# Kernel tuning notes

Measured on AMD Instinct MI355X. Metric: run time of the kernel, lower is better.

The kernel has to match this reference:

```python
import jax, jax.numpy as jnp
import numpy as np

B, S, D = 4, 2048, 512
H, DK, DV = 8, 64, 64
DFF = 2048
LN_EPS = 1e-5


def _layernorm(x, g, b):
    mu = jnp.mean(x, axis=-1, keepdims=True)
    var = jnp.mean(jnp.square(x - mu), axis=-1, keepdims=True)
    return (x - mu) * jax.lax.rsqrt(var + LN_EPS) * g + b


def setup_inputs() -> dict:
    key = jax.random.key(0)
    ks = jax.random.split(key, 9)
    def xavier(k, shape):
        fan_out, fan_in = shape
        std = np.sqrt(2.0 / (fan_in + fan_out))
        return jax.random.normal(k, shape, jnp.float32) * std
    GELU_GAIN = 1.85
    return {
        "x": jax.random.normal(ks[0], (B, S, D), jnp.float32),
        "attention_mask": jax.random.randint(ks[1], (B, S), 0, 2).astype(bool),
        "Wq": xavier(ks[2], (H * DK, D)),
        "Wk": xavier(ks[3], (H * DK, D)),
        "Wv": xavier(ks[4], (H * DV, D)),
        "Wp": xavier(ks[5], (D, H * DV)),
        "W1": xavier(ks[6], (DFF, D)) * GELU_GAIN,
        "b1": jnp.zeros((DFF,), jnp.float32),
        "W2": xavier(ks[7], (D, DFF)),
        "b2": jnp.zeros((D,), jnp.float32),
        "ln1_g": jnp.ones((D,), jnp.float32),
        "ln1_b": jnp.zeros((D,), jnp.float32),
        "ln2_g": jnp.ones((D,), jnp.float32),
        "ln2_b": jnp.zeros((D,), jnp.float32),
    }


def reference(x, attention_mask, Wq, Wk, Wv, Wp, W1, b1, W2, b2,
              ln1_g, ln1_b, ln2_g, ln2_b):
    b, s, d = x.shape
    residual = x
    q = (x @ Wq.T).reshape(b, s, H, DK)  # [B,S,H,DK]
    k = (x @ Wk.T).reshape(b, s, H, DK)
    v = (x @ Wv.T).reshape(b, s, H, DV)
    score = jnp.einsum("bshd,bthd->bhst", q, k) * (DK ** -0.5)  # [B,H,S,S]
    # subtractive mask: score -= 100 * not(mask)
    score = score - 100.0 * (~attention_mask)[:, None, None, :].astype(score.dtype)
    p = jax.nn.softmax(score, axis=-1)
    ctx = jnp.einsum("bhst,bthd->bshd", p, v).reshape(b, s, H * DV)
    att = ctx @ Wp.T  # dropout p=0.1 is identity in eval
    h = _layernorm(att + residual, ln1_g, ln1_b)
    ff = jax.nn.gelu(h @ W1.T + b1, approximate=False) @ W2.T + b2
    out = _layernorm(ff + h, ln2_g, ln2_b)
    return out
```

## Files before the change

kernel.cpp:

```cpp
#include <hip/hip_runtime.h>
#include <cstdint>
#include <cstddef>

#define B_ 4
#define S_ 2048
#define D_ 512
#define H_ 8
#define DK_ 64
#define DFF_ 2048

using s16x8  = __attribute__((ext_vector_type(8))) short;
using bf16x8 = __attribute__((ext_vector_type(8))) __bf16;
using f32x4  = __attribute__((ext_vector_type(4))) float;

__device__ __forceinline__ short f2bf(float f) {
  unsigned u = __builtin_bit_cast(unsigned, f);
  u += 0x7FFFu + ((u >> 16) & 1u);
  return (short)(u >> 16);
}
__device__ __forceinline__ float bf2f(short s) {
  unsigned u = ((unsigned)(unsigned short)s) << 16;
  return __builtin_bit_cast(float, u);
}

__device__ __forceinline__ void gl2lds16(const void* g, void* l) {
  __builtin_amdgcn_global_load_lds(
      (const __attribute__((address_space(1))) void*)g,
      (__attribute__((address_space(3))) void*)l, 16, 0, 0);
}

__global__ __launch_bounds__(256)
void cvt_all(const float* __restrict__ x, const float* __restrict__ Wq,
             const float* __restrict__ Wk, const float* __restrict__ Wv,
             const float* __restrict__ Wp, const float* __restrict__ W1,
             const float* __restrict__ W2,
             short* __restrict__ xb, short* __restrict__ wqkv,
             short* __restrict__ wp, short* __restrict__ w1, short* __restrict__ w2) {
  int blk = blockIdx.x;
  const float* src; short* dst; int off;
  if (blk < 4096)      { src = x;  dst = xb;            off = blk; }
  else if (blk < 4352) { src = Wq; dst = wqkv;          off = blk - 4096; }
  else if (blk < 4608) { src = Wk; dst = wqkv + 262144; off = blk - 4352; }
  else if (blk < 4864) { src = Wv; dst = wqkv + 524288; off = blk - 4608; }
  else if (blk < 5120) { src = Wp; dst = wp;            off = blk - 4864; }
  else if (blk < 6144) { src = W1; dst = w1;            off = blk - 5120; }
  else                 { src = W2; dst = w2;            off = blk - 6144; }
  int i = (off * 256 + threadIdx.x) * 4;
  float4 v = *(const float4*)(src + i);
  *(short4*)(dst + i) = make_short4(f2bf(v.x), f2bf(v.y), f2bf(v.z), f2bf(v.w));
}

__global__ __launch_bounds__(256) void mask_detect(const unsigned* __restrict__ m,
                                                   unsigned* __restrict__ flag) {
  int i = blockIdx.x * 256 + threadIdx.x;
  unsigned v = m[i];
  if (v) atomicOr(flag, v);
}

__global__ __launch_bounds__(256) void mask_convert(const void* __restrict__ m,
                                                    const unsigned* __restrict__ flag,
                                                    float* __restrict__ mb) {
  int i = blockIdx.x * 256 + threadIdx.x;
  unsigned f = *flag;
  int v;
  if ((f & ~1u) == 0u)            v = ((const int*)m)[i];
  else if (f == 0x3F800000u)      v = (((const float*)m)[i] != 0.0f);
  else                            v = ((const unsigned char*)m)[i];
  mb[i] = v ? 0.0f : -100.0f;
}

constexpr int BM = 128, BN = 128, BK = 32;

template <int MODE>
__global__ __launch_bounds__(256)
void gemm_bt(const short* __restrict__ A, const short* __restrict__ B,
             int M, int N, int K,
             const float* __restrict__ aux1,
             void* __restrict__ out0, void* __restrict__ out1, void* __restrict__ out2) {
  __shared__ alignas(16) short As[BM][BK];
  __shared__ alignas(16) short Bs[BN][BK];

  const int tid  = threadIdx.x;
  const int lane = tid & 63;
  const int wave = tid >> 6;
  const int quad = lane >> 4;
  const int l16  = lane & 15;
  const int wm   = (wave >> 1) * 64;
  const int wn   = (wave & 1) * 64;
  const int bm   = blockIdx.x * BM;
  const int bn   = blockIdx.y * BN;

  const short* Ag = A + (size_t)(bm + wave * 32 + (lane >> 2)) * K + (lane & 3) * 8;
  const short* Bg = B + (size_t)(bn + wave * 32 + (lane >> 2)) * K + (lane & 3) * 8;
  short* AsW = &As[wave * 32][0];
  short* BsW = &Bs[wave * 32][0];
  const size_t row16 = (size_t)16 * K;

  f32x4 acc[4][4] = {};

  for (int k0 = 0; k0 < K; k0 += BK) {
    gl2lds16(Ag + k0,          AsW);
    gl2lds16(Ag + k0 + row16,  AsW + 16 * BK);
    gl2lds16(Bg + k0,          BsW);
    gl2lds16(Bg + k0 + row16,  BsW + 16 * BK);
    __syncthreads();

    bf16x8 a[4], b[4];
#pragma unroll
    for (int i = 0; i < 4; ++i)
      a[i] = __builtin_bit_cast(bf16x8, *(const s16x8*)&As[wm + i * 16 + l16][quad * 8]);
#pragma unroll
    for (int j = 0; j < 4; ++j)
      b[j] = __builtin_bit_cast(bf16x8, *(const s16x8*)&Bs[wn + j * 16 + l16][quad * 8]);
#pragma unroll
    for (int i = 0; i < 4; ++i)
#pragma unroll
      for (int j = 0; j < 4; ++j)
        acc[i][j] = __builtin_amdgcn_mfma_f32_16x16x32_bf16(a[i], b[j], acc[i][j], 0, 0, 0);
    __syncthreads();
  }

#pragma unroll
  for (int i = 0; i < 4; ++i) {
    const int m0 = bm + wm + i * 16 + quad * 4;
#pragma unroll
    for (int j = 0; j < 4; ++j) {
      const int n = bn + wn + j * 16 + l16;
      if constexpr (MODE == 0) {
        const int bb = m0 >> 11, ss0 = m0 & 2047;
        if (n < 512) {
          short4 pk = make_short4(f2bf(acc[i][j][0] * 0.125f), f2bf(acc[i][j][1] * 0.125f),
                                  f2bf(acc[i][j][2] * 0.125f), f2bf(acc[i][j][3] * 0.125f));
          *(short4*)((short*)out0 +
              ((((size_t)bb * H_ + (n >> 6)) * 64 + (n & 63)) * S_ + ss0)) = pk;
        } else if (n >= 1024) {
          const int nn = n - 1024;
          short4 pk = make_short4(f2bf(acc[i][j][0]), f2bf(acc[i][j][1]),
                                  f2bf(acc[i][j][2]), f2bf(acc[i][j][3]));
          *(short4*)((short*)out2 +
              ((((size_t)bb * H_ + (nn >> 6)) * 64 + (nn & 63)) * S_ + ss0)) = pk;
        } else {
          const int nn = n - 512;
          const int hh = nn >> 6, dd = nn & 63;
          const size_t rowb = ((size_t)bb * H_ + hh) * S_ + ss0;
#pragma unroll
          for (int rr = 0; rr < 4; ++rr)
            ((short*)out1)[(rowb + rr) * 64 + dd] = f2bf(acc[i][j][rr]);
        }
      } else {
#pragma unroll
        for (int rr = 0; rr < 4; ++rr) {
          float t = acc[i][j][rr] + aux1[n];
          float gl = 0.5f * t * (1.0f + erff(t * 0.70710678118f));
          ((short*)out0)[(size_t)(m0 + rr) * N + n] = f2bf(gl);
        }
      }
    }
  }
}

__global__ __launch_bounds__(128)
void gemm_bt2_sk(const short* __restrict__ A, const short* __restrict__ B,
                 int M, int N, int K, float* __restrict__ outp) {
  __shared__ alignas(16) short As[128][32];
  __shared__ alignas(16) short Bs[64][32];

  const int tid  = threadIdx.x;
  const int lane = tid & 63;
  const int wave = tid >> 6;
  const int quad = lane >> 4;
  const int l16  = lane & 15;
  const int wm   = wave * 64;
  const int bm   = blockIdx.x * 128;
  const int bn   = blockIdx.y * 64;
  const int Kh   = K >> 1;
  const int koff = blockIdx.z * Kh;

  const int srow = wave * 16 + (lane >> 2);
  const int scol = (lane & 3) * 8;
  const short* Ag = A + (size_t)(bm + srow) * K + koff + scol;
  const short* Bg = B + (size_t)(bn + srow) * K + koff + scol;
  short* AsW = &As[wave * 16][0];
  short* BsW = &Bs[wave * 16][0];
  const size_t row32 = (size_t)32 * K;

  f32x4 acc[4][4] = {};

  for (int k0 = 0; k0 < Kh; k0 += 32) {
    gl2lds16(Ag + k0,              AsW);
    gl2lds16(Ag + k0 + row32,      AsW + 32 * 32);
    gl2lds16(Ag + k0 + 2 * row32,  AsW + 64 * 32);
    gl2lds16(Ag + k0 + 3 * row32,  AsW + 96 * 32);
    gl2lds16(Bg + k0,              BsW);
    gl2lds16(Bg + k0 + row32,      BsW + 32 * 32);
    __syncthreads();

    bf16x8 a[4], b[4];
#pragma unroll
    for (int i = 0; i < 4; ++i)
      a[i] = __builtin_bit_cast(bf16x8, *(const s16x8*)&As[wm + i * 16 + l16][quad * 8]);
#pragma unroll
    for (int j = 0; j < 4; ++j)
      b[j] = __builtin_bit_cast(bf16x8, *(const s16x8*)&Bs[j * 16 + l16][quad * 8]);
#pragma unroll
    for (int i = 0; i < 4; ++i)
#pragma unroll
      for (int j = 0; j < 4; ++j)
        acc[i][j] = __builtin_amdgcn_mfma_f32_16x16x32_bf16(a[i], b[j], acc[i][j], 0, 0, 0);
    __syncthreads();
  }

  float* dst = outp + (size_t)blockIdx.z * M * N;
#pragma unroll
  for (int i = 0; i < 4; ++i) {
    const int m0 = bm + wm + i * 16 + quad * 4;
#pragma unroll
    for (int j = 0; j < 4; ++j) {
      const int n = bn + j * 16 + l16;
#pragma unroll
      for (int rr = 0; rr < 4; ++rr)
        dst[(size_t)(m0 + rr) * N + n] = acc[i][j][rr];
    }
  }
}

__global__ __launch_bounds__(256)
void flash_attn_mfma(const short* __restrict__ QTg, const short* __restrict__ Kb,
                     const short* __restrict__ Vtg, const float* __restrict__ maskbias,
                     short* __restrict__ ctxb) {
  __shared__ alignas(16) short Ks[64][72];
  __shared__ alignas(16) short Vt[64][72];
  __shared__ alignas(16) short Ps[4][32][72];
  __shared__ alignas(16) float mrow[S_];

  const int b = blockIdx.z, h = blockIdx.y;
  const int tid = threadIdx.x;
  const int w = tid >> 6, lane = tid & 63;
  const int quad = lane >> 4, l16 = lane & 15;
  const size_t base  = ((size_t)(b * H_ + h)) * S_ * DK_;
  const size_t baseT = ((size_t)(b * H_ + h)) * DK_ * S_;
  const int q0 = blockIdx.x * 128;

  {
    const float4* mp = (const float4*)(maskbias + (size_t)b * S_);
    ((float4*)mrow)[tid]       = mp[tid];
    ((float4*)mrow)[tid + 256] = mp[tid + 256];
  }

  bf16x8 qa[2][2];
#pragma unroll
  for (int st = 0; st < 2; ++st) {
    const int q = q0 + w * 32 + st * 16 + l16;
#pragma unroll
    for (int c = 0; c < 2; ++c) {
      s16x8 t;
#pragma unroll
      for (int j = 0; j < 8; ++j)
        t[j] = QTg[baseT + (size_t)(c * 32 + quad * 8 + j) * S_ + q];
      qa[st][c] = __builtin_bit_cast(bf16x8, t);
    }
  }

  f32x4 Oc[2][4] = {};
  float li[2][4] = {};

  const int r = tid >> 2, c16 = (tid & 3) * 16;
  const short* kp = Kb  + base  + (size_t)r * 64 + c16;
  const short* vp = Vtg + baseT + (size_t)r * S_ + c16;

  s16x8 kr0 = *(const s16x8*)(kp);
  s16x8 kr1 = *(const s16x8*)(kp + 8);
  s16x8 vr0 = *(const s16x8*)(vp);
  s16x8 vr1 = *(const s16x8*)(vp + 8);

  for (int t0 = 0; t0 < S_; t0 += 64) {
    __syncthreads();
    *(s16x8*)&Ks[r][c16]     = kr0;
    *(s16x8*)&Ks[r][c16 + 8] = kr1;
    *(s16x8*)&Vt[r][c16]     = vr0;
    *(s16x8*)&Vt[r][c16 + 8] = vr1;
    __syncthreads();

    if (t0 + 64 < S_) {
      kr0 = *(const s16x8*)(kp + (size_t)(t0 + 64) * 64);
      kr1 = *(const s16x8*)(kp + (size_t)(t0 + 64) * 64 + 8);
      vr0 = *(const s16x8*)(vp + t0 + 64);
      vr1 = *(const s16x8*)(vp + t0 + 64 + 8);
    }

    f32x4 sc[2][4] = {};
#pragma unroll
    for (int c = 0; c < 2; ++c) {
#pragma unroll
      for (int jt = 0; jt < 4; ++jt) {
        bf16x8 kb = __builtin_bit_cast(bf16x8,
            *(const s16x8*)&Ks[jt * 16 + l16][c * 32 + quad * 8]);
        sc[0][jt] = __builtin_amdgcn_mfma_f32_16x16x32_bf16(qa[0][c], kb, sc[0][jt], 0, 0, 0);
        sc[1][jt] = __builtin_amdgcn_mfma_f32_16x16x32_bf16(qa[1][c], kb, sc[1][jt], 0, 0, 0);
      }
    }

    float mb4[4];
#pragma unroll
    for (int jt = 0; jt < 4; ++jt) mb4[jt] = mrow[t0 + jt * 16 + l16];
#pragma unroll
    for (int st = 0; st < 2; ++st) {
#pragma unroll
      for (int jt = 0; jt < 4; ++jt) {
#pragma unroll
        for (int rr = 0; rr < 4; ++rr) {
          float p = __expf(sc[st][jt][rr] + mb4[jt]);
          unsigned u = __builtin_bit_cast(unsigned, p) & 0xFFFF0000u;
          li[st][rr] += __builtin_bit_cast(float, u);
          Ps[w][st * 16 + quad * 4 + rr][jt * 16 + l16] = (short)(u >> 16);
        }
      }
    }

#pragma unroll
    for (int c = 0; c < 2; ++c) {
      bf16x8 pa0 = __builtin_bit_cast(bf16x8,
          *(const s16x8*)&Ps[w][l16][c * 32 + quad * 8]);
      bf16x8 pa1 = __builtin_bit_cast(bf16x8,
          *(const s16x8*)&Ps[w][16 + l16][c * 32 + quad * 8]);
#pragma unroll
      for (int dt = 0; dt < 4; ++dt) {
        bf16x8 vb = __builtin_bit_cast(bf16x8,
            *(const s16x8*)&Vt[dt * 16 + l16][c * 32 + quad * 8]);
        Oc[0][dt] = __builtin_amdgcn_mfma_f32_16x16x32_bf16(pa0, vb, Oc[0][dt], 0, 0, 0);
        Oc[1][dt] = __builtin_amdgcn_mfma_f32_16x16x32_bf16(pa1, vb, Oc[1][dt], 0, 0, 0);
      }
    }
  }

#pragma unroll
  for (int st = 0; st < 2; ++st) {
#pragma unroll
    for (int rr = 0; rr < 4; ++rr) {
      float l = li[st][rr];
#pragma unroll
      for (int m = 1; m < 16; m <<= 1) l += __shfl_xor(l, m);
      float inv = 1.f / l;
      const size_t row = (size_t)b * S_ + q0 + w * 32 + st * 16 + quad * 4 + rr;
#pragma unroll
      for (int dt = 0; dt < 4; ++dt)
        ctxb[row * (H_ * DK_) + h * 64 + dt * 16 + l16] = f2bf(Oc[st][dt][rr] * inv);
    }
  }
}

__global__ __launch_bounds__(256)
void ln_fused(const float* __restrict__ p0, const float* __restrict__ p1,
              const float* __restrict__ xres, const short* __restrict__ hres,
              const float* __restrict__ bias,
              const float* __restrict__ g, const float* __restrict__ bb,
              float* __restrict__ out32, short* __restrict__ outb) {
  const int wave = threadIdx.x >> 6, lane = threadIdx.x & 63;
  const int token = blockIdx.x * 4 + wave;
  const size_t off = (size_t)token * D_;
  const int c = lane * 8;

  float v[8];
  {
    float4 a0 = *(const float4*)(p0 + off + c);
    float4 a1 = *(const float4*)(p0 + off + c + 4);
    float4 b0 = *(const float4*)(p1 + off + c);
    float4 b1 = *(const float4*)(p1 + off + c + 4);
    v[0]=a0.x+b0.x; v[1]=a0.y+b0.y; v[2]=a0.z+b0.z; v[3]=a0.w+b0.w;
    v[4]=a1.x+b1.x; v[5]=a1.y+b1.y; v[6]=a1.z+b1.z; v[7]=a1.w+b1.w;
  }
  if (xres) {
    float4 x0 = *(const float4*)(xres + off + c);
    float4 x1 = *(const float4*)(xres + off + c + 4);
    v[0]+=x0.x; v[1]+=x0.y; v[2]+=x0.z; v[3]+=x0.w;
    v[4]+=x1.x; v[5]+=x1.y; v[6]+=x1.z; v[7]+=x1.w;
  }
  if (hres) {
    short4 h0 = *(const short4*)(hres + off + c);
    short4 h1 = *(const short4*)(hres + off + c + 4);
    v[0]+=bf2f(h0.x); v[1]+=bf2f(h0.y); v[2]+=bf2f(h0.z); v[3]+=bf2f(h0.w);
    v[4]+=bf2f(h1.x); v[5]+=bf2f(h1.y); v[6]+=bf2f(h1.z); v[7]+=bf2f(h1.w);
  }
  if (bias) {
    float4 c0 = *(const float4*)(bias + c);
    float4 c1 = *(const float4*)(bias + c + 4);
    v[0]+=c0.x; v[1]+=c0.y; v[2]+=c0.z; v[3]+=c0.w;
    v[4]+=c1.x; v[5]+=c1.y; v[6]+=c1.z; v[7]+=c1.w;
  }

  float sum = 0.f;
#pragma unroll
  for (int i = 0; i < 8; ++i) sum += v[i];
#pragma unroll
  for (int m = 1; m < 64; m <<= 1) sum += __shfl_xor(sum, m);
  float mu = sum * (1.0f / D_);
  float vs = 0.f;
#pragma unroll
  for (int i = 0; i < 8; ++i) { v[i] -= mu; vs += v[i] * v[i]; }
#pragma unroll
  for (int m = 1; m < 64; m <<= 1) vs += __shfl_xor(vs, m);
  float rstd = rsqrtf(vs * (1.0f / D_) + 1e-5f);
#pragma unroll
  for (int i = 0; i < 8; ++i) {
    float val = v[i] * rstd * g[c + i] + bb[c + i];
    if (out32) out32[off + c + i] = val;
    if (outb)  outb[off + c + i] = f2bf(val);
  }
}

constexpr size_t OFF_XB   = 0;
constexpr size_t OFF_WQKV = 8388608;
constexpr size_t OFF_WP   = 9961472;
constexpr size_t OFF_W1   = 10485760;
constexpr size_t OFF_W2   = 12582912;
constexpr size_t OFF_QT   = 14680064;
constexpr size_t OFF_K    = 23068672;
constexpr size_t OFF_VT   = 31457280;
constexpr size_t OFF_CTX  = 39845888;
constexpr size_t OFF_P0   = 48234496;
constexpr size_t OFF_P1   = 65011712;
constexpr size_t OFF_HB   = 81788928;
constexpr size_t OFF_FF1  = 14680064;
constexpr size_t OFF_MB   = 90177536;
constexpr size_t OFF_FLAG = 90210304;
constexpr size_t WS_NEED  = 90210308;

extern "C" void kernel_launch(void* const* d_in, const int* in_sizes, int n_in,
                              void* d_out, int out_size, void* d_ws, size_t ws_size,
                              hipStream_t stream) {
  if (ws_size < WS_NEED) return;

  const float* x    = (const float*)d_in[0];
  const void*  msk  = d_in[1];
  const float* Wq   = (const float*)d_in[2];
  const float* Wk   = (const float*)d_in[3];
  const float* Wv   = (const float*)d_in[4];
  const float* Wp   = (const float*)d_in[5];
  const float* W1   = (const float*)d_in[6];
  const float* b1   = (const float*)d_in[7];
  const float* W2   = (const float*)d_in[8];
  const float* b2   = (const float*)d_in[9];
  const float* ln1g = (const float*)d_in[10];
  const float* ln1b = (const float*)d_in[11];
  const float* ln2g = (const float*)d_in[12];
  const float* ln2b = (const float*)d_in[13];

  char* ws = (char*)d_ws;
  short* xb    = (short*)(ws + OFF_XB);
  short* wqkv  = (short*)(ws + OFF_WQKV);
  short* Wpb   = (short*)(ws + OFF_WP);
  short* W1b   = (short*)(ws + OFF_W1);
  short* W2b   = (short*)(ws + OFF_W2);
  short* QTb   = (short*)(ws + OFF_QT);
  short* Kbh   = (short*)(ws + OFF_K);
  short* VTb   = (short*)(ws + OFF_VT);
  short* ctxb  = (short*)(ws + OFF_CTX);
  float* p0    = (float*)(ws + OFF_P0);
  short* hb    = (short*)(ws + OFF_HB);
  short* ff1b  = (short*)(ws + OFF_FF1);
  float* mbias = (float*)(ws + OFF_MB);
  unsigned* flag = (unsigned*)(ws + OFF_FLAG);

  hipMemsetAsync(flag, 0, 4, stream);
  mask_detect<<<8, 256, 0, stream>>>((const unsigned*)msk, flag);
  mask_convert<<<32, 256, 0, stream>>>(msk, flag, mbias);

  cvt_all<<<7168, 256, 0, stream>>>(x, Wq, Wk, Wv, Wp, W1, W2,
                                    xb, wqkv, Wpb, W1b, W2b);

  gemm_bt<0><<<dim3(64, 12), 256, 0, stream>>>(xb, wqkv, 8192, 1536, 512,
                                               nullptr, QTb, Kbh, VTb);

  flash_attn_mfma<<<dim3(S_ / 128, H_, B_), 256, 0, stream>>>(QTb, Kbh, VTb, mbias, ctxb);

  gemm_bt2_sk<<<dim3(64, 8, 2), 128, 0, stream>>>(ctxb, Wpb, 8192, 512, 512, p0);

  ln_fused<<<2048, 256, 0, stream>>>(p0, p0 + (size_t)8192 * 512, x, nullptr, nullptr,
                                     ln1g, ln1b, nullptr, hb);

  gemm_bt<2><<<dim3(64, 16), 256, 0, stream>>>(hb, W1b, 8192, 2048, 512,
                                               b1, ff1b, nullptr, nullptr);

  gemm_bt2_sk<<<dim3(64, 8, 2), 128, 0, stream>>>(ff1b, W2b, 8192, 512, 2048, p0);

  ln_fused<<<2048, 256, 0, stream>>>(p0, p0 + (size_t)8192 * 512, nullptr, hb, b2,
                                     ln2g, ln2b, (float*)d_out, nullptr);
}
```

Before: 340.8 us.

## Widen GEMM K-tile with XOR-swizzled LDS and unify split-K GEMMs; fuse mask kernels

Measured after the change: 325.0 us. 1.05x faster.

```diff
diff --git a/kernel.cpp b/kernel.cpp
--- a/kernel.cpp
+++ b/kernel.cpp
@@ -50,26 +50,26 @@
   *(short4*)(dst + i) = make_short4(f2bf(v.x), f2bf(v.y), f2bf(v.z), f2bf(v.w));
 }
 
-__global__ __launch_bounds__(256) void mask_detect(const unsigned* __restrict__ m,
-                                                   unsigned* __restrict__ flag) {
-  int i = blockIdx.x * 256 + threadIdx.x;
-  unsigned v = m[i];
-  if (v) atomicOr(flag, v);
-}
-
-__global__ __launch_bounds__(256) void mask_convert(const void* __restrict__ m,
-                                                    const unsigned* __restrict__ flag,
-                                                    float* __restrict__ mb) {
-  int i = blockIdx.x * 256 + threadIdx.x;
-  unsigned f = *flag;
-  int v;
-  if ((f & ~1u) == 0u)            v = ((const int*)m)[i];
-  else if (f == 0x3F800000u)      v = (((const float*)m)[i] != 0.0f);
-  else                            v = ((const unsigned char*)m)[i];
-  mb[i] = v ? 0.0f : -100.0f;
-}
-
-constexpr int BM = 128, BN = 128, BK = 32;
+__global__ __launch_bounds__(256)
+void mask_all(const void* __restrict__ m, float* __restrict__ mb) {
+  __shared__ unsigned red[4];
+  const unsigned* mw = (const unsigned*)m;
+  const int t = threadIdx.x;
+  unsigned v = 0;
+#pragma unroll
+  for (int i = 0; i < 8; ++i) v |= mw[t + i * 256];
+#pragma unroll
+  for (int s = 1; s < 64; s <<= 1) v |= __shfl_xor(v, s);
+  if ((t & 63) == 0) red[t >> 6] = v;
+  __syncthreads();
+  unsigned f = red[0] | red[1] | red[2] | red[3];
+  int i = blockIdx.x * 256 + t;
+  int val;
+  if ((f & ~1u) == 0u)            val = ((const int*)m)[i];
+  else if (f == 0x3F800000u)      val = (((const float*)m)[i] != 0.0f);
+  else                            val = ((const unsigned char*)m)[i];
+  mb[i] = val ? 0.0f : -100.0f;
+}
 
 template <int MODE>
 __global__ __launch_bounds__(256)
@@ -77,8 +77,8 @@
              int M, int N, int K,
              const float* __restrict__ aux1,
              void* __restrict__ out0, void* __restrict__ out1, void* __restrict__ out2) {
-  __shared__ alignas(16) short As[BM][BK];
-  __shared__ alignas(16) short Bs[BN][BK];
+  __shared__ alignas(16) short As[128][64];
+  __shared__ alignas(16) short Bs[128][64];
 
   const int tid  = threadIdx.x;
   const int lane = tid & 63;
@@ -87,36 +87,47 @@
   const int l16  = lane & 15;
   const int wm   = (wave >> 1) * 64;
   const int wn   = (wave & 1) * 64;
-  const int bm   = blockIdx.x * BM;
-  const int bn   = blockIdx.y * BN;
-
-  const short* Ag = A + (size_t)(bm + wave * 32 + (lane >> 2)) * K + (lane & 3) * 8;
-  const short* Bg = B + (size_t)(bn + wave * 32 + (lane >> 2)) * K + (lane & 3) * 8;
-  short* AsW = &As[wave * 32][0];
-  short* BsW = &Bs[wave * 32][0];
-  const size_t row16 = (size_t)16 * K;
+  const int bm   = blockIdx.x * 128;
+  const int bn   = blockIdx.y * 128;
+  const int Kh   = K / gridDim.z;
+  const int koff = blockIdx.z * Kh;
+
+  const int srow8 = lane >> 3;
+  const int pb    = lane & 7;
 
   f32x4 acc[4][4] = {};
 
-  for (int k0 = 0; k0 < K; k0 += BK) {
-    gl2lds16(Ag + k0,          AsW);
-    gl2lds16(Ag + k0 + row16,  AsW + 16 * BK);
-    gl2lds16(Bg + k0,          BsW);
-    gl2lds16(Bg + k0 + row16,  BsW + 16 * BK);
+  for (int k0 = 0; k0 < Kh; k0 += 64) {
+#pragma unroll
+    for (int i = 0; i < 4; ++i) {
+      const int rr = wave * 32 + i * 8 + srow8;
+      const int cb = pb ^ (rr & 7);
+      gl2lds16(A + (size_t)(bm + rr) * K + koff + k0 + cb * 8, &As[wave * 32 + i * 8][0]);
+      gl2lds16(B + (size_t)(bn + rr) * K + koff + k0 + cb * 8, &Bs[wave * 32 + i * 8][0]);
+    }
     __syncthreads();
 
-    bf16x8 a[4], b[4];
-#pragma unroll
-    for (int i = 0; i < 4; ++i)
-      a[i] = __builtin_bit_cast(bf16x8, *(const s16x8*)&As[wm + i * 16 + l16][quad * 8]);
-#pragma unroll
-    for (int j = 0; j < 4; ++j)
-      b[j] = __builtin_bit_cast(bf16x8, *(const s16x8*)&Bs[wn + j * 16 + l16][quad * 8]);
-#pragma unroll
-    for (int i = 0; i < 4; ++i)
-#pragma unroll
-      for (int j = 0; j < 4; ++j)
-        acc[i][j] = __builtin_amdgcn_mfma_f32_16x16x32_bf16(a[i], b[j], acc[i][j], 0, 0, 0);
+#pragma unroll
+    for (int c = 0; c < 2; ++c) {
+      bf16x8 a[4], b[4];
+#pragma unroll
+      for (int i = 0; i < 4; ++i) {
+        const int row = wm + i * 16 + l16;
+        const int pba = (c * 4 + quad) ^ (row & 7);
+        a[i] = __builtin_bit_cast(bf16x8, *(const s16x8*)&As[row][pba * 8]);
+      }
+#pragma unroll
+      for (int j = 0; j < 4; ++j) {
+        const int row = wn + j * 16 + l16;
+        const int pbb = (c * 4 + quad) ^ (row & 7);
+        b[j] = __builtin_bit_cast(bf16x8, *(const s16x8*)&Bs[row][pbb * 8]);
+      }
+#pragma unroll
+      for (int i = 0; i < 4; ++i)
+#pragma unroll
+        for (int j = 0; j < 4; ++j)
+          acc[i][j] = __builtin_amdgcn_mfma_f32_16x16x32_bf16(a[i], b[j], acc[i][j], 0, 0, 0);
+    }
     __syncthreads();
   }
 
@@ -141,12 +152,16 @@
               ((((size_t)bb * H_ + (nn >> 6)) * 64 + (nn & 63)) * S_ + ss0)) = pk;
         } else {
           const int nn = n - 512;
-          const int hh = nn >> 6, dd = nn & 63;
-          const size_t rowb = ((size_t)bb * H_ + hh) * S_ + ss0;
+          const size_t rowb = ((size_t)bb * H_ + (nn >> 6)) * S_ + ss0;
 #pragma unroll
           for (int rr = 0; rr < 4; ++rr)
-            ((short*)out1)[(rowb + rr) * 64 + dd] = f2bf(acc[i][j][rr]);
+            ((short*)out1)[(rowb + rr) * 64 + (nn & 63)] = f2bf(acc[i][j][rr]);
         }
+      } else if constexpr (MODE == 1) {
+        float* dst = (float*)out0 + (size_t)blockIdx.z * M * N;
+#pragma unroll
+        for (int rr = 0; rr < 4; ++rr)
+          dst[(size_t)(m0 + rr) * N + n] = acc[i][j][rr];
       } else {
 #pragma unroll
         for (int rr = 0; rr < 4; ++rr) {
@@ -155,71 +170,6 @@
           ((short*)out0)[(size_t)(m0 + rr) * N + n] = f2bf(gl);
         }
       }
-    }
-  }
-}
-
-__global__ __launch_bounds__(128)
-void gemm_bt2_sk(const short* __restrict__ A, const short* __restrict__ B,
-                 int M, int N, int K, float* __restrict__ outp) {
-  __shared__ alignas(16) short As[128][32];
-  __shared__ alignas(16) short Bs[64][32];
-
-  const int tid  = threadIdx.x;
-  const int lane = tid & 63;
-  const int wave = tid >> 6;
-  const int quad = lane >> 4;
-  const int l16  = lane & 15;
-  const int wm   = wave * 64;
-  const int bm   = blockIdx.x * 128;
-  const int bn   = blockIdx.y * 64;
-  const int Kh   = K >> 1;
-  const int koff = blockIdx.z * Kh;
-
-  const int srow = wave * 16 + (lane >> 2);
-  const int scol = (lane & 3) * 8;
-  const short* Ag = A + (size_t)(bm + srow) * K + koff + scol;
-  const short* Bg = B + (size_t)(bn + srow) * K + koff + scol;
-  short* AsW = &As[wave * 16][0];
-  short* BsW = &Bs[wave * 16][0];
-  const size_t row32 = (size_t)32 * K;
-
-  f32x4 acc[4][4] = {};
-
-  for (int k0 = 0; k0 < Kh; k0 += 32) {
-    gl2lds16(Ag + k0,              AsW);
-    gl2lds16(Ag + k0 + row32,      AsW + 32 * 32);
-    gl2lds16(Ag + k0 + 2 * row32,  AsW + 64 * 32);
-    gl2lds16(Ag + k0 + 3 * row32,  AsW + 96 * 32);
-    gl2lds16(Bg + k0,              BsW);
-    gl2lds16(Bg + k0 + row32,      BsW + 32 * 32);
-    __syncthreads();
-
-    bf16x8 a[4], b[4];
-#pragma unroll
-    for (int i = 0; i < 4; ++i)
-      a[i] = __builtin_bit_cast(bf16x8, *(const s16x8*)&As[wm + i * 16 + l16][quad * 8]);
-#pragma unroll
-    for (int j = 0; j < 4; ++j)
-      b[j] = __builtin_bit_cast(bf16x8, *(const s16x8*)&Bs[j * 16 + l16][quad * 8]);
-#pragma unroll
-    for (int i = 0; i < 4; ++i)
-#pragma unroll
-      for (int j = 0; j < 4; ++j)
-        acc[i][j] = __builtin_amdgcn_mfma_f32_16x16x32_bf16(a[i], b[j], acc[i][j], 0, 0, 0);
-    __syncthreads();
-  }
-
-  float* dst = outp + (size_t)blockIdx.z * M * N;
-#pragma unroll
-  for (int i = 0; i < 4; ++i) {
-    const int m0 = bm + wm + i * 16 + quad * 4;
-#pragma unroll
-    for (int j = 0; j < 4; ++j) {
-      const int n = bn + j * 16 + l16;
-#pragma unroll
-      for (int rr = 0; rr < 4; ++rr)
-        dst[(size_t)(m0 + rr) * N + n] = acc[i][j][rr];
     }
   }
 }
@@ -422,8 +372,7 @@
 constexpr size_t OFF_HB   = 81788928;
 constexpr size_t OFF_FF1  = 14680064;
 constexpr size_t OFF_MB   = 90177536;
-constexpr size_t OFF_FLAG = 90210304;
-constexpr size_t WS_NEED  = 90210308;
+constexpr size_t WS_NEED  = 90210304;
 
 extern "C" void kernel_launch(void* const* d_in, const int* in_sizes, int n_in,
                               void* d_out, int out_size, void* d_ws, size_t ws_size,
@@ -459,29 +408,28 @@
   short* hb    = (short*)(ws + OFF_HB);
   short* ff1b  = (short*)(ws + OFF_FF1);
   float* mbias = (float*)(ws + OFF_MB);
-  unsigned* flag = (unsigned*)(ws + OFF_FLAG);
-
-  hipMemsetAsync(flag, 0, 4, stream);
-  mask_detect<<<8, 256, 0, stream>>>((const unsigned*)msk, flag);
-  mask_convert<<<32, 256, 0, stream>>>(msk, flag, mbias);
+
+  mask_all<<<32, 256, 0, stream>>>(msk, mbias);
 
   cvt_all<<<7168, 256, 0, stream>>>(x, Wq, Wk, Wv, Wp, W1, W2,
                                     xb, wqkv, Wpb, W1b, W2b);
 
-  gemm_bt<0><<<dim3(64, 12), 256, 0, stream>>>(xb, wqkv, 8192, 1536, 512,
-                                               nullptr, QTb, Kbh, VTb);
+  gemm_bt<0><<<dim3(64, 12, 1), 256, 0, stream>>>(xb, wqkv, 8192, 1536, 512,
+                                                  nullptr, QTb, Kbh, VTb);
 
   flash_attn_mfma<<<dim3(S_ / 128, H_, B_), 256, 0, stream>>>(QTb, Kbh, VTb, mbias, ctxb);
 
-  gemm_bt2_sk<<<dim3(64, 8, 2), 128, 0, stream>>>(ctxb, Wpb, 8192, 512, 512, p0);
+  gemm_bt<1><<<dim3(64, 4, 2), 256, 0, stream>>>(ctxb, Wpb, 8192, 512, 512,
+                                                 nullptr, p0, nullptr, nullptr);
 
   ln_fused<<<2048, 256, 0, stream>>>(p0, p0 + (size_t)8192 * 512, x, nullptr, nullptr,
                                      ln1g, ln1b, nullptr, hb);
 
-  gemm_bt<2><<<dim3(64, 16), 256, 0, stream>>>(hb, W1b, 8192, 2048, 512,
-                                               b1, ff1b, nullptr, nullptr);
-
-  gemm_bt2_sk<<<dim3(64, 8, 2), 128, 0, stream>>>(ff1b, W2b, 8192, 512, 2048, p0);
+  gemm_bt<2><<<dim3(64, 16, 1), 256, 0, stream>>>(hb, W1b, 8192, 2048, 512,
+                                                  b1, ff1b, nullptr, nullptr);
+
+  gemm_bt<1><<<dim3(64, 4, 2), 256, 0, stream>>>(ff1b, W2b, 8192, 512, 2048,
+                                                 nullptr, p0, nullptr, nullptr);
 
   ln_fused<<<2048, 256, 0, stream>>>(p0, p0 + (size_t)8192 * 512, nullptr, hb, b2,
                                      ln2g, ln2b, (float*)d_out, nullptr);
```
